# Kernel optimization log

Measured on AMD Instinct MI355X. Metric: run time of the kernel, lower is better.

The kernel has to match this reference:

```python
import jax, jax.numpy as jnp
import numpy as np

DIM = 256
NUM_HEADS = 8
WS = 8
HEAD_DIM = DIM // NUM_HEADS
N = WS * WS
B_NW = 8192


def _relative_position_index():
    coords = np.stack(np.meshgrid(np.arange(WS), np.arange(WS), indexing='ij')).reshape(2, -1)  # [2, N]
    rel = coords[:, :, None] - coords[:, None, :]           # [2, N, N]
    rel = rel.transpose(1, 2, 0)                            # [N, N, 2]
    rel[:, :, 0] += WS - 1
    rel[:, :, 1] += WS - 1
    rel[:, :, 0] *= 2 * WS - 1
    return rel.sum(-1).astype(np.int32)                     # [N, N]


def setup_inputs() -> dict:
    key = jax.random.key(0)
    ks = jax.random.split(key, 6)
    x = jax.random.normal(ks[0], (B_NW, N, DIM), dtype=jnp.float32)
    qkv_w = jax.random.normal(ks[1], (3 * DIM, DIM), dtype=jnp.float32) * (DIM ** -0.5)
    qkv_b = jnp.zeros((3 * DIM,), dtype=jnp.float32)
    proj_w = jax.random.normal(ks[2], (DIM, DIM), dtype=jnp.float32) * (DIM ** -0.5)
    proj_b = jnp.zeros((DIM,), dtype=jnp.float32)
    rel_bias_table = jax.random.normal(ks[3], ((2 * WS - 1) ** 2, NUM_HEADS), dtype=jnp.float32) * 0.02
    rel_pos_index = jnp.asarray(_relative_position_index())
    return {"x": x, "qkv_w": qkv_w, "qkv_b": qkv_b, "proj_w": proj_w,
            "proj_b": proj_b, "rel_bias_table": rel_bias_table,
            "rel_pos_index": rel_pos_index}


def reference(x, qkv_w, qkv_b, proj_w, proj_b, rel_bias_table, rel_pos_index):
    B, Nn, C = x.shape
    scale = HEAD_DIM ** -0.5
    qkv = x @ qkv_w.T + qkv_b                                # [B, N, 3C]
    qkv = qkv.reshape(B, Nn, 3, NUM_HEADS, HEAD_DIM)
    q = qkv[:, :, 0].transpose(0, 2, 1, 3)                   # [B, H, N, d]
    k = qkv[:, :, 1].transpose(0, 2, 1, 3)
    v = qkv[:, :, 2].transpose(0, 2, 1, 3)
    attn = jnp.einsum('bhnd,bhmd->bhnm', q, k) * scale       # [B, H, N, N]
    bias = rel_bias_table[rel_pos_index.reshape(-1)].reshape(Nn, Nn, NUM_HEADS)
    attn = attn + bias.transpose(2, 0, 1)[None]              # add [1, H, N, N]
    attn = jax.nn.softmax(attn, axis=-1)
    out = jnp.einsum('bhnm,bhmd->bhnd', attn, v)             # [B, H, N, d]
    out = out.transpose(0, 2, 1, 3).reshape(B, Nn, C)
    return out @ proj_w.T + proj_b
```

## Files before the change

kernel.cpp:

```cpp
#include <hip/hip_runtime.h>
#include <stdint.h>


typedef __attribute__((ext_vector_type(8))) short bf16x8;
typedef __attribute__((ext_vector_type(4))) float f32x4;

#define QK_LD 520
#define VT_LD 72
#define P_LD  72
#define X_LD  264
#define SMEM_ELEMS (64 * QK_LD + 256 * VT_LD + 2 * 64 * P_LD + 64 * X_LD)
#define SMEM_BYTES (SMEM_ELEMS * 2)

__device__ __forceinline__ unsigned short f2bf(float x) {
  union { float f; unsigned int u; } v; v.f = x;
  return (unsigned short)((v.u + 0x7fffu + ((v.u >> 16) & 1u)) >> 16);
}
__device__ __forceinline__ float bf2f(unsigned short u) {
  union { unsigned int u; float f; } v; v.u = ((unsigned int)u) << 16;
  return v.f;
}

__global__ void prep_kernel(const float* __restrict__ qkv_w,
                            const float* __restrict__ proj_w,
                            const float* __restrict__ table,
                            const int* __restrict__ idx,
                            unsigned short* __restrict__ wq,
                            unsigned short* __restrict__ wp,
                            unsigned short* __restrict__ bm) {
  int i = blockIdx.x * 256 + threadIdx.x;
  if (i < 196608) {
    wq[i] = f2bf(qkv_w[i]);
  } else if (i < 262144) {
    int j = i - 196608;
    wp[j] = f2bf(proj_w[j]);
  } else {
    int k = i - 262144;
    int h = k >> 12;
    int rc = k & 4095;
    bm[k] = f2bf(table[idx[rc] * 8 + h]);
  }
}

__launch_bounds__(512, 2)
__global__ void lewin_kernel(const float* __restrict__ x,
                             const unsigned short* __restrict__ wq,
                             const float* __restrict__ qkv_b,
                             const unsigned short* __restrict__ wp,
                             const float* __restrict__ proj_b,
                             const unsigned short* __restrict__ bm,
                             float* __restrict__ out) {
  extern __shared__ __align__(16) unsigned short smem[];
  unsigned short* sQK = smem;
  unsigned short* sVT = smem + 64 * QK_LD;
  unsigned short* sP  = sVT + 256 * VT_LD;
  unsigned short* sX  = sP + 2 * 64 * P_LD;

  const int b    = blockIdx.x;
  const int tid  = threadIdx.x;
  const int wv   = tid >> 6;
  const int lane = tid & 63;
  const int l16  = lane & 15;
  const int quad = lane >> 4;
  const f32x4 fz = {0.0f, 0.0f, 0.0f, 0.0f};

  const float* xb = x + (size_t)b * 16384;
  #pragma unroll
  for (int it = 0; it < 8; ++it) {
    int f = (it * 512 + tid) * 4;
    float4 v = *(const float4*)(xb + f);
    int row = f >> 8, col = f & 255;
    ushort4 u;
    u.x = f2bf(v.x); u.y = f2bf(v.y); u.z = f2bf(v.z); u.w = f2bf(v.w);
    *(ushort4*)(sX + row * X_LD + col) = u;
  }
  __syncthreads();

  bf16x8 afrag[4][8];
  #pragma unroll
  for (int m = 0; m < 4; ++m)
    #pragma unroll
    for (int kk = 0; kk < 8; ++kk)
      afrag[m][kk] = *(const bf16x8*)(sX + (16 * m + l16) * X_LD + kk * 32 + quad * 8);

  #pragma unroll
  for (int nt = 0; nt < 6; ++nt) {
    int col = wv * 96 + nt * 16 + l16;
    bf16x8 bfrag[8];
    const unsigned short* wrow = wq + (size_t)col * 256 + quad * 8;
    #pragma unroll
    for (int kk = 0; kk < 8; ++kk)
      bfrag[kk] = *(const bf16x8*)(wrow + kk * 32);
    f32x4 acc[4] = {fz, fz, fz, fz};
    #pragma unroll
    for (int kk = 0; kk < 8; ++kk)
      #pragma unroll
      for (int m = 0; m < 4; ++m)
        acc[m] = __builtin_amdgcn_mfma_f32_16x16x32_bf16(afrag[m][kk], bfrag[kk], acc[m], 0, 0, 0);
    float bc = qkv_b[col];
    #pragma unroll
    for (int m = 0; m < 4; ++m) {
      int row0 = 16 * m + quad * 4;
      if (col < 512) {
        #pragma unroll
        for (int r = 0; r < 4; ++r)
          sQK[(row0 + r) * QK_LD + col] = f2bf(acc[m][r] + bc);
      } else {
        int c = col - 512;
        ushort4 u;
        u.x = f2bf(acc[m][0] + bc); u.y = f2bf(acc[m][1] + bc);
        u.z = f2bf(acc[m][2] + bc); u.w = f2bf(acc[m][3] + bc);
        *(ushort4*)(sVT + c * VT_LD + row0) = u;
      }
    }
  }
  __syncthreads();

  const int mt = wv & 3;
  const int hs = wv >> 2;
  unsigned short* sOut = sX;
  unsigned short* myP = sP + hs * (64 * P_LD);
  const float scale = 0.17677669529663687f;
  const float log2e = 1.4426950408889634f;

  #pragma unroll
  for (int hh = 0; hh < 4; ++hh) {
    int h = hs * 4 + hh;
    bf16x8 qa = *(const bf16x8*)(sQK + (16 * mt + l16) * QK_LD + h * 32 + quad * 8);
    float lg[4][4];
    #pragma unroll
    for (int nt = 0; nt < 4; ++nt) {
      bf16x8 kb = *(const bf16x8*)(sQK + (nt * 16 + l16) * QK_LD + 256 + h * 32 + quad * 8);
      f32x4 a = fz;
      a = __builtin_amdgcn_mfma_f32_16x16x32_bf16(qa, kb, a, 0, 0, 0);
      const unsigned short* bmr = bm + (h * 64 + 16 * mt + quad * 4) * 64 + nt * 16 + l16;
      #pragma unroll
      for (int r = 0; r < 4; ++r)
        lg[nt][r] = a[r] * scale + bf2f(bmr[r * 64]);
    }
    #pragma unroll
    for (int r = 0; r < 4; ++r) {
      float m0 = fmaxf(fmaxf(lg[0][r], lg[1][r]), fmaxf(lg[2][r], lg[3][r]));
      #pragma unroll
      for (int s = 1; s < 16; s <<= 1) m0 = fmaxf(m0, __shfl_xor(m0, s, 64));
      float e0 = exp2f((lg[0][r] - m0) * log2e);
      float e1 = exp2f((lg[1][r] - m0) * log2e);
      float e2 = exp2f((lg[2][r] - m0) * log2e);
      float e3 = exp2f((lg[3][r] - m0) * log2e);
      float sum = e0 + e1 + e2 + e3;
      #pragma unroll
      for (int s = 1; s < 16; s <<= 1) sum += __shfl_xor(sum, s, 64);
      float inv = 1.0f / sum;
      unsigned short* pd = myP + (16 * mt + quad * 4 + r) * P_LD + l16;
      pd[0]  = f2bf(e0 * inv);
      pd[16] = f2bf(e1 * inv);
      pd[32] = f2bf(e2 * inv);
      pd[48] = f2bf(e3 * inv);
    }
    f32x4 o0 = fz, o1 = fz;
    #pragma unroll
    for (int kk = 0; kk < 2; ++kk) {
      bf16x8 pa  = *(const bf16x8*)(myP + (16 * mt + l16) * P_LD + kk * 32 + quad * 8);
      bf16x8 vb0 = *(const bf16x8*)(sVT + (h * 32 + l16) * VT_LD + kk * 32 + quad * 8);
      bf16x8 vb1 = *(const bf16x8*)(sVT + (h * 32 + 16 + l16) * VT_LD + kk * 32 + quad * 8);
      o0 = __builtin_amdgcn_mfma_f32_16x16x32_bf16(pa, vb0, o0, 0, 0, 0);
      o1 = __builtin_amdgcn_mfma_f32_16x16x32_bf16(pa, vb1, o1, 0, 0, 0);
    }
    #pragma unroll
    for (int r = 0; r < 4; ++r) {
      int orow = 16 * mt + quad * 4 + r;
      sOut[orow * X_LD + h * 32 + l16]      = f2bf(o0[r]);
      sOut[orow * X_LD + h * 32 + 16 + l16] = f2bf(o1[r]);
    }
  }
  __syncthreads();

  bf16x8 of[4][8];
  #pragma unroll
  for (int m = 0; m < 4; ++m)
    #pragma unroll
    for (int kk = 0; kk < 8; ++kk)
      of[m][kk] = *(const bf16x8*)(sOut + (16 * m + l16) * X_LD + kk * 32 + quad * 8);

  float* ob = out + (size_t)b * 16384;
  #pragma unroll
  for (int nt = 0; nt < 2; ++nt) {
    int col = wv * 32 + nt * 16 + l16;
    bf16x8 bfrag[8];
    const unsigned short* wrow = wp + (size_t)col * 256 + quad * 8;
    #pragma unroll
    for (int kk = 0; kk < 8; ++kk)
      bfrag[kk] = *(const bf16x8*)(wrow + kk * 32);
    f32x4 acc[4] = {fz, fz, fz, fz};
    #pragma unroll
    for (int kk = 0; kk < 8; ++kk)
      #pragma unroll
      for (int m = 0; m < 4; ++m)
        acc[m] = __builtin_amdgcn_mfma_f32_16x16x32_bf16(of[m][kk], bfrag[kk], acc[m], 0, 0, 0);
    float pb = proj_b[col];
    #pragma unroll
    for (int m = 0; m < 4; ++m)
      #pragma unroll
      for (int r = 0; r < 4; ++r)
        ob[(16 * m + quad * 4 + r) * 256 + col] = acc[m][r] + pb;
  }
}

extern "C" void kernel_launch(void* const* d_in, const int* in_sizes, int n_in,
                              void* d_out, int out_size, void* d_ws, size_t ws_size,
                              hipStream_t stream) {
  const float* x      = (const float*)d_in[0];
  const float* qkv_w  = (const float*)d_in[1];
  const float* qkv_b  = (const float*)d_in[2];
  const float* proj_w = (const float*)d_in[3];
  const float* proj_b = (const float*)d_in[4];
  const float* table  = (const float*)d_in[5];
  const int*   idx    = (const int*)d_in[6];
  float* out = (float*)d_out;

  unsigned short* wq = (unsigned short*)d_ws;
  unsigned short* wp = wq + 196608;
  unsigned short* bm = wp + 65536;

  (void)hipFuncSetAttribute((const void*)lewin_kernel,
                            hipFuncAttributeMaxDynamicSharedMemorySize, SMEM_BYTES);

  prep_kernel<<<1152, 256, 0, stream>>>(qkv_w, proj_w, table, idx, wq, wp, bm);
  lewin_kernel<<<8192, 512, SMEM_BYTES, stream>>>(x, wq, qkv_b, wp, proj_b, bm, out);
}
```

Before: 1.599 ms.

## Use 1024-thread blocks, drop softmax max pass, defer normalization, swizzle P buffer

The fused window-attention kernel now runs 16 waves per block instead of 8, so each wave covers fewer QKV columns, heads and projection columns, and register fragments are loaded per k-step rather than held whole. Softmax skips the max-subtraction pass: log2e is folded into the bias table and the score scale, exp2 and rcp use hardware intrinsics, and the 1/sum factor is applied after the PV product. The P buffer reuses the x staging area with an XOR swizzle instead of padding, and the attention output goes into the QK region, cutting shared memory. Dropping max subtraction risks overflow on large logits, and the extra waves change register pressure and scheduling.

Result: faster. 1.416 ms (-11.4%).

```diff
diff --git a/kernel.cpp b/kernel.cpp
--- a/kernel.cpp
+++ b/kernel.cpp
@@ -1,4 +1,5 @@
 #include <hip/hip_runtime.h>
+#include <hip/hip_bf16.h>
 #include <stdint.h>
 
 
@@ -7,14 +8,17 @@
 
 #define QK_LD 520
 #define VT_LD 72
-#define P_LD  72
 #define X_LD  264
-#define SMEM_ELEMS (64 * QK_LD + 256 * VT_LD + 2 * 64 * P_LD + 64 * X_LD)
+#define SQK_ELEMS (64 * QK_LD)
+#define SVT_ELEMS (256 * VT_LD)
+#define SX_ELEMS  (64 * X_LD)
+#define SMEM_ELEMS (SQK_ELEMS + SVT_ELEMS + SX_ELEMS)
 #define SMEM_BYTES (SMEM_ELEMS * 2)
 
 __device__ __forceinline__ unsigned short f2bf(float x) {
-  union { float f; unsigned int u; } v; v.f = x;
-  return (unsigned short)((v.u + 0x7fffu + ((v.u >> 16) & 1u)) >> 16);
+  union { __hip_bfloat16 h; unsigned short u; } c;
+  c.h = __float2bfloat16(x);
+  return c.u;
 }
 __device__ __forceinline__ float bf2f(unsigned short u) {
   union { unsigned int u; float f; } v; v.u = ((unsigned int)u) << 16;
@@ -38,11 +42,11 @@
     int k = i - 262144;
     int h = k >> 12;
     int rc = k & 4095;
-    bm[k] = f2bf(table[idx[rc] * 8 + h]);
-  }
-}
-
-__launch_bounds__(512, 2)
+    bm[k] = f2bf(table[idx[rc] * 8 + h] * 1.4426950408889634f);
+  }
+}
+
+__launch_bounds__(1024, 4)
 __global__ void lewin_kernel(const float* __restrict__ x,
                              const unsigned short* __restrict__ wq,
                              const float* __restrict__ qkv_b,
@@ -52,9 +56,8 @@
                              float* __restrict__ out) {
   extern __shared__ __align__(16) unsigned short smem[];
   unsigned short* sQK = smem;
-  unsigned short* sVT = smem + 64 * QK_LD;
-  unsigned short* sP  = sVT + 256 * VT_LD;
-  unsigned short* sX  = sP + 2 * 64 * P_LD;
+  unsigned short* sVT = smem + SQK_ELEMS;
+  unsigned short* sX  = sVT + SVT_ELEMS;
 
   const int b    = blockIdx.x;
   const int tid  = threadIdx.x;
@@ -66,8 +69,8 @@
 
   const float* xb = x + (size_t)b * 16384;
   #pragma unroll
-  for (int it = 0; it < 8; ++it) {
-    int f = (it * 512 + tid) * 4;
+  for (int it = 0; it < 4; ++it) {
+    int f = (it * 1024 + tid) * 4;
     float4 v = *(const float4*)(xb + f);
     int row = f >> 8, col = f & 255;
     ushort4 u;
@@ -76,134 +79,129 @@
   }
   __syncthreads();
 
-  bf16x8 afrag[4][8];
-  #pragma unroll
-  for (int m = 0; m < 4; ++m)
-    #pragma unroll
-    for (int kk = 0; kk < 8; ++kk)
-      afrag[m][kk] = *(const bf16x8*)(sX + (16 * m + l16) * X_LD + kk * 32 + quad * 8);
-
-  #pragma unroll
-  for (int nt = 0; nt < 6; ++nt) {
-    int col = wv * 96 + nt * 16 + l16;
-    bf16x8 bfrag[8];
-    const unsigned short* wrow = wq + (size_t)col * 256 + quad * 8;
-    #pragma unroll
-    for (int kk = 0; kk < 8; ++kk)
-      bfrag[kk] = *(const bf16x8*)(wrow + kk * 32);
-    f32x4 acc[4] = {fz, fz, fz, fz};
-    #pragma unroll
-    for (int kk = 0; kk < 8; ++kk)
+  {
+    f32x4 acc[3][4];
+    #pragma unroll
+    for (int nt = 0; nt < 3; ++nt)
+      #pragma unroll
+      for (int m = 0; m < 4; ++m) acc[nt][m] = fz;
+    const int colb = wv * 48;
+    #pragma unroll
+    for (int kk = 0; kk < 8; ++kk) {
+      bf16x8 a[4];
       #pragma unroll
       for (int m = 0; m < 4; ++m)
-        acc[m] = __builtin_amdgcn_mfma_f32_16x16x32_bf16(afrag[m][kk], bfrag[kk], acc[m], 0, 0, 0);
-    float bc = qkv_b[col];
-    #pragma unroll
-    for (int m = 0; m < 4; ++m) {
-      int row0 = 16 * m + quad * 4;
-      if (col < 512) {
+        a[m] = *(const bf16x8*)(sX + (16 * m + l16) * X_LD + kk * 32 + quad * 8);
+      #pragma unroll
+      for (int nt = 0; nt < 3; ++nt) {
+        bf16x8 bg = *(const bf16x8*)(wq + (size_t)(colb + nt * 16 + l16) * 256 + kk * 32 + quad * 8);
         #pragma unroll
-        for (int r = 0; r < 4; ++r)
-          sQK[(row0 + r) * QK_LD + col] = f2bf(acc[m][r] + bc);
-      } else {
-        int c = col - 512;
-        ushort4 u;
-        u.x = f2bf(acc[m][0] + bc); u.y = f2bf(acc[m][1] + bc);
-        u.z = f2bf(acc[m][2] + bc); u.w = f2bf(acc[m][3] + bc);
-        *(ushort4*)(sVT + c * VT_LD + row0) = u;
+        for (int m = 0; m < 4; ++m)
+          acc[nt][m] = __builtin_amdgcn_mfma_f32_16x16x32_bf16(a[m], bg, acc[nt][m], 0, 0, 0);
       }
     }
+    #pragma unroll
+    for (int nt = 0; nt < 3; ++nt) {
+      int col = colb + nt * 16 + l16;
+      float bc = qkv_b[col];
+      #pragma unroll
+      for (int m = 0; m < 4; ++m) {
+        int row0 = 16 * m + quad * 4;
+        if (col < 512) {
+          #pragma unroll
+          for (int r = 0; r < 4; ++r)
+            sQK[(row0 + r) * QK_LD + col] = f2bf(acc[nt][m][r] + bc);
+        } else {
+          int c = col - 512;
+          ushort4 u;
+          u.x = f2bf(acc[nt][m][0] + bc); u.y = f2bf(acc[nt][m][1] + bc);
+          u.z = f2bf(acc[nt][m][2] + bc); u.w = f2bf(acc[nt][m][3] + bc);
+          *(ushort4*)(sVT + c * VT_LD + row0) = u;
+        }
+      }
+    }
   }
   __syncthreads();
 
   const int mt = wv & 3;
-  const int hs = wv >> 2;
-  unsigned short* sOut = sX;
-  unsigned short* myP = sP + hs * (64 * P_LD);
-  const float scale = 0.17677669529663687f;
-  const float log2e = 1.4426950408889634f;
-
-  #pragma unroll
-  for (int hh = 0; hh < 4; ++hh) {
-    int h = hs * 4 + hh;
+  const int hp = wv >> 2;
+  unsigned short* sP = sX + hp * 4096;
+  const float s2 = 0.17677669529663687f * 1.4426950408889634f;
+  f32x4 o[2][2] = {{fz, fz}, {fz, fz}};
+  float inv[2][4];
+
+  #pragma unroll
+  for (int hh = 0; hh < 2; ++hh) {
+    int h = hp * 2 + hh;
     bf16x8 qa = *(const bf16x8*)(sQK + (16 * mt + l16) * QK_LD + h * 32 + quad * 8);
-    float lg[4][4];
+    float e[4][4];
     #pragma unroll
     for (int nt = 0; nt < 4; ++nt) {
       bf16x8 kb = *(const bf16x8*)(sQK + (nt * 16 + l16) * QK_LD + 256 + h * 32 + quad * 8);
-      f32x4 a = fz;
-      a = __builtin_amdgcn_mfma_f32_16x16x32_bf16(qa, kb, a, 0, 0, 0);
+      f32x4 a = __builtin_amdgcn_mfma_f32_16x16x32_bf16(qa, kb, fz, 0, 0, 0);
       const unsigned short* bmr = bm + (h * 64 + 16 * mt + quad * 4) * 64 + nt * 16 + l16;
       #pragma unroll
       for (int r = 0; r < 4; ++r)
-        lg[nt][r] = a[r] * scale + bf2f(bmr[r * 64]);
+        e[nt][r] = __builtin_amdgcn_exp2f(fmaf(a[r], s2, bf2f(bmr[r * 64])));
     }
     #pragma unroll
     for (int r = 0; r < 4; ++r) {
-      float m0 = fmaxf(fmaxf(lg[0][r], lg[1][r]), fmaxf(lg[2][r], lg[3][r]));
-      #pragma unroll
-      for (int s = 1; s < 16; s <<= 1) m0 = fmaxf(m0, __shfl_xor(m0, s, 64));
-      float e0 = exp2f((lg[0][r] - m0) * log2e);
-      float e1 = exp2f((lg[1][r] - m0) * log2e);
-      float e2 = exp2f((lg[2][r] - m0) * log2e);
-      float e3 = exp2f((lg[3][r] - m0) * log2e);
-      float sum = e0 + e1 + e2 + e3;
-      #pragma unroll
-      for (int s = 1; s < 16; s <<= 1) sum += __shfl_xor(sum, s, 64);
-      float inv = 1.0f / sum;
-      unsigned short* pd = myP + (16 * mt + quad * 4 + r) * P_LD + l16;
-      pd[0]  = f2bf(e0 * inv);
-      pd[16] = f2bf(e1 * inv);
-      pd[32] = f2bf(e2 * inv);
-      pd[48] = f2bf(e3 * inv);
-    }
-    f32x4 o0 = fz, o1 = fz;
+      float s = (e[0][r] + e[1][r]) + (e[2][r] + e[3][r]);
+      #pragma unroll
+      for (int sft = 1; sft < 16; sft <<= 1) s += __shfl_xor(s, sft, 64);
+      inv[hh][r] = __builtin_amdgcn_rcpf(s);
+      int row = 16 * mt + quad * 4 + r;
+      int swz = (row & 7) << 3;
+      unsigned short* pd = sP + row * 64;
+      pd[(l16 + 0) ^ swz]  = f2bf(e[0][r]);
+      pd[(l16 + 16) ^ swz] = f2bf(e[1][r]);
+      pd[(l16 + 32) ^ swz] = f2bf(e[2][r]);
+      pd[(l16 + 48) ^ swz] = f2bf(e[3][r]);
+    }
+    int prow = 16 * mt + l16;
+    int pswz = (prow & 7) << 3;
     #pragma unroll
     for (int kk = 0; kk < 2; ++kk) {
-      bf16x8 pa  = *(const bf16x8*)(myP + (16 * mt + l16) * P_LD + kk * 32 + quad * 8);
+      bf16x8 pa  = *(const bf16x8*)(sP + prow * 64 + ((kk * 32 + quad * 8) ^ pswz));
       bf16x8 vb0 = *(const bf16x8*)(sVT + (h * 32 + l16) * VT_LD + kk * 32 + quad * 8);
       bf16x8 vb1 = *(const bf16x8*)(sVT + (h * 32 + 16 + l16) * VT_LD + kk * 32 + quad * 8);
-      o0 = __builtin_amdgcn_mfma_f32_16x16x32_bf16(pa, vb0, o0, 0, 0, 0);
-      o1 = __builtin_amdgcn_mfma_f32_16x16x32_bf16(pa, vb1, o1, 0, 0, 0);
-    }
+      o[hh][0] = __builtin_amdgcn_mfma_f32_16x16x32_bf16(pa, vb0, o[hh][0], 0, 0, 0);
+      o[hh][1] = __builtin_amdgcn_mfma_f32_16x16x32_bf16(pa, vb1, o[hh][1], 0, 0, 0);
+    }
+  }
+  __syncthreads();
+
+  unsigned short* sOut = sQK;
+  #pragma unroll
+  for (int hh = 0; hh < 2; ++hh) {
+    int h = hp * 2 + hh;
     #pragma unroll
     for (int r = 0; r < 4; ++r) {
       int orow = 16 * mt + quad * 4 + r;
-      sOut[orow * X_LD + h * 32 + l16]      = f2bf(o0[r]);
-      sOut[orow * X_LD + h * 32 + 16 + l16] = f2bf(o1[r]);
-    }
-  }
-  __syncthreads();
-
-  bf16x8 of[4][8];
+      sOut[orow * X_LD + h * 32 + l16]      = f2bf(o[hh][0][r] * inv[hh][r]);
+      sOut[orow * X_LD + h * 32 + 16 + l16] = f2bf(o[hh][1][r] * inv[hh][r]);
+    }
+  }
+  __syncthreads();
+
+  float* ob = out + (size_t)b * 16384;
+  const int col = wv * 16 + l16;
+  f32x4 acc[4] = {fz, fz, fz, fz};
+  #pragma unroll
+  for (int kk = 0; kk < 8; ++kk) {
+    bf16x8 bg = *(const bf16x8*)(wp + (size_t)col * 256 + kk * 32 + quad * 8);
+    #pragma unroll
+    for (int m = 0; m < 4; ++m) {
+      bf16x8 a = *(const bf16x8*)(sOut + (16 * m + l16) * X_LD + kk * 32 + quad * 8);
+      acc[m] = __builtin_amdgcn_mfma_f32_16x16x32_bf16(a, bg, acc[m], 0, 0, 0);
+    }
+  }
+  float pb = proj_b[col];
   #pragma unroll
   for (int m = 0; m < 4; ++m)
     #pragma unroll
-    for (int kk = 0; kk < 8; ++kk)
-      of[m][kk] = *(const bf16x8*)(sOut + (16 * m + l16) * X_LD + kk * 32 + quad * 8);
-
-  float* ob = out + (size_t)b * 16384;
-  #pragma unroll
-  for (int nt = 0; nt < 2; ++nt) {
-    int col = wv * 32 + nt * 16 + l16;
-    bf16x8 bfrag[8];
-    const unsigned short* wrow = wp + (size_t)col * 256 + quad * 8;
-    #pragma unroll
-    for (int kk = 0; kk < 8; ++kk)
-      bfrag[kk] = *(const bf16x8*)(wrow + kk * 32);
-    f32x4 acc[4] = {fz, fz, fz, fz};
-    #pragma unroll
-    for (int kk = 0; kk < 8; ++kk)
-      #pragma unroll
-      for (int m = 0; m < 4; ++m)
-        acc[m] = __builtin_amdgcn_mfma_f32_16x16x32_bf16(of[m][kk], bfrag[kk], acc[m], 0, 0, 0);
-    float pb = proj_b[col];
-    #pragma unroll
-    for (int m = 0; m < 4; ++m)
-      #pragma unroll
-      for (int r = 0; r < 4; ++r)
-        ob[(16 * m + quad * 4 + r) * 256 + col] = acc[m][r] + pb;
-  }
+    for (int r = 0; r < 4; ++r)
+      ob[(16 * m + quad * 4 + r) * 256 + col] = acc[m][r] + pb;
 }
 
 extern "C" void kernel_launch(void* const* d_in, const int* in_sizes, int n_in,
@@ -226,5 +224,5 @@
                             hipFuncAttributeMaxDynamicSharedMemorySize, SMEM_BYTES);
 
   prep_kernel<<<1152, 256, 0, stream>>>(qkv_w, proj_w, table, idx, wq, wp, bm);
-  lewin_kernel<<<8192, 512, SMEM_BYTES, stream>>>(x, wq, qkv_b, wp, proj_b, bm, out);
-}
+  lewin_kernel<<<8192, 1024, SMEM_BYTES, stream>>>(x, wq, qkv_b, wp, proj_b, bm, out);
+}
```
